# Kernel optimization log

Measured on AMD Instinct MI355X. Metric: run time of the kernel, lower is better.

Reference implementation:

```python
import jax, jax.numpy as jnp
import numpy as np

NUM_REGIONS = 32  # region ids 1..32; id 0 is background, excluded like torch.unique()[ids>0]


def setup_inputs() -> dict:
    key = jax.random.key(0)
    k1, k2 = jax.random.split(key)
    B, T, C, D, H, W = 2, 8, 64, 48, 48, 48
    features = jax.random.normal(k1, (B, T, C, D, H, W), dtype=jnp.float32)
    segmentation = jax.random.randint(k2, (B, 1, D, H, W), 0, NUM_REGIONS + 1, dtype=jnp.int32)
    return {"features": features, "segmentation": segmentation}


def reference(features, segmentation):
    # features: [B, T, C, D, H, W], segmentation: [B, 1, D, H, W] (int region ids)
    B, T, C, D, H, W = features.shape
    N = D * H * W
    seg = segmentation.reshape(B, N)                 # [B, N]
    feats = features.reshape(B, T, C, N)             # [B, T, C, N]

    def per_batch(f, s):
        # f: [T, C, N], s: [N]
        fv = f.reshape(T * C, N).T                   # [N, T*C] voxel-major
        sums = jax.ops.segment_sum(fv, s, num_segments=NUM_REGIONS + 1)          # [R+1, T*C]
        counts = jax.ops.segment_sum(jnp.ones((N,), f.dtype), s,
                                     num_segments=NUM_REGIONS + 1)               # [R+1]
        # mean per region; empty regions stay zero (torch code `continue`s, leaving zeros)
        means = jnp.where(counts[:, None] > 0,
                          sums / jnp.maximum(counts, 1.0)[:, None],
                          0.0)
        return means[1:].reshape(NUM_REGIONS, T, C).transpose(1, 0, 2)           # [T, R, C]

    return jax.vmap(per_batch)(feats, seg)          # [B, T, num_regions, feature_dim]
```

## Files before the change

kernel.cpp:

```cpp
#include <hip/hip_runtime.h>


#define BB 2
#define TT 8
#define CC 64
#define NVOX 110592
#define NREG 32
#define RS 33
#define ACC (RS*CC)
#define CHUNKV 1024
#define VPW (CHUNKV/4)

__global__ __launch_bounds__(256) void seg_hist(const int* __restrict__ seg,
                                                float* __restrict__ counts) {
    __shared__ float h[4 * RS];
    const int tid = threadIdx.x;
    const int w = tid >> 6;
    for (int i = tid; i < 4 * RS; i += 256) h[i] = 0.f;
    __syncthreads();

    const int base = blockIdx.x * 1024 + tid * 4;
    const int b = base / NVOX;
    const int4 s4 = *(const int4*)(seg + base);
    atomicAdd(&h[w * RS + s4.x], 1.f);
    atomicAdd(&h[w * RS + s4.y], 1.f);
    atomicAdd(&h[w * RS + s4.z], 1.f);
    atomicAdd(&h[w * RS + s4.w], 1.f);
    __syncthreads();

    if (tid < RS) {
        const float v = h[tid] + h[RS + tid] + h[2 * RS + tid] + h[3 * RS + tid];
        atomicAdd(&counts[b * RS + tid], v);
    }
}

__global__ __launch_bounds__(256) void seg_sum(const float* __restrict__ feat,
                                               const int* __restrict__ seg,
                                               float* __restrict__ out) {
    __shared__ float s[4 * ACC];
    const int tid = threadIdx.x;
    const int w = tid >> 6;
    const int lane = tid & 63;
    const int b = blockIdx.z;
    const int t = blockIdx.y;

    float* __restrict__ acc = s + w * ACC;
    for (int i = lane; i < ACC; i += 64) acc[i] = 0.f;

    const int v0 = blockIdx.x * CHUNKV + w * VPW;
    const float* __restrict__ fb =
        feat + ((size_t)(b * TT + t) * CC + lane) * NVOX;
    const int* __restrict__ sb = seg + (size_t)b * NVOX;

    #pragma unroll 4
    for (int g = 0; g < VPW; g += 4) {
        const int v = v0 + g;
        const int4 sv = *(const int4*)(sb + v);
        const float4 f = *(const float4*)(fb + v);
        acc[sv.x * CC + lane] += f.x;
        acc[sv.y * CC + lane] += f.y;
        acc[sv.z * CC + lane] += f.z;
        acc[sv.w * CC + lane] += f.w;
    }
    __syncthreads();

    float* __restrict__ outbt = out + (size_t)(b * TT + t) * NREG * CC;
    for (int i = tid; i < NREG * CC; i += 256) {
        const int off = ((i >> 6) + 1) * CC + (i & 63);
        const float v = s[off] + s[ACC + off] + s[2 * ACC + off] + s[3 * ACC + off];
        atomicAdd(&outbt[i], v);
    }
}

__global__ __launch_bounds__(256) void seg_div(float* __restrict__ out,
                                               const float* __restrict__ counts) {
    const int i = blockIdx.x * 256 + threadIdx.x;
    const int b = i >> 14;
    const int r = ((i >> 6) & 31) + 1;
    const float cnt = counts[b * RS + r];
    const float v = out[i];
    out[i] = cnt > 0.f ? v / cnt : 0.f;
}

extern "C" void kernel_launch(void* const* d_in, const int* in_sizes, int n_in,
                              void* d_out, int out_size, void* d_ws, size_t ws_size,
                              hipStream_t stream) {
    const float* feat = (const float*)d_in[0];
    const int* seg = (const int*)d_in[1];
    float* out = (float*)d_out;
    float* counts = (float*)d_ws;

    hipMemsetAsync(d_out, 0, (size_t)out_size * sizeof(float), stream);
    hipMemsetAsync(d_ws, 0, (size_t)(BB * RS) * sizeof(float), stream);

    seg_hist<<<dim3((BB * NVOX) / 1024), 256, 0, stream>>>(seg, counts);
    seg_sum<<<dim3(NVOX / CHUNKV, TT, BB), 256, 0, stream>>>(feat, seg, out);
    seg_div<<<dim3(out_size / 256), 256, 0, stream>>>(out, counts);
}
```

Before: 614.1 us.

## Coalesce feature loads via per-wave LDS transpose tile in segment sum

Each wave now loads 16 consecutive voxels for 16 channels at a time, with 4 lanes per channel, so global reads become contiguous segments instead of one strided row per lane. The values are transposed through a padded per-wave LDS tile, then accumulated into the per-region LDS histogram as before. This targets poor memory coalescing in the bandwidth-bound reduction. The cost is extra LDS traffic and more shared memory per block, which may reduce occupancy.

```diff
diff --git a/kernel.cpp b/kernel.cpp
--- a/kernel.cpp
+++ b/kernel.cpp
@@ -7,9 +7,12 @@
 #define NVOX 110592
 #define NREG 32
 #define RS 33
-#define ACC (RS*CC)
+#define TS 67
+#define WTILE (16*TS)
+#define WACC (RS*CC)
+#define WLDS (WTILE+WACC)
+#define VPW 256
 #define CHUNKV 1024
-#define VPW (CHUNKV/4)
 
 __global__ __launch_bounds__(256) void seg_hist(const int* __restrict__ seg,
                                                 float* __restrict__ counts) {
@@ -37,37 +40,67 @@
 __global__ __launch_bounds__(256) void seg_sum(const float* __restrict__ feat,
                                                const int* __restrict__ seg,
                                                float* __restrict__ out) {
-    __shared__ float s[4 * ACC];
+    __shared__ float s[4 * WLDS];
     const int tid = threadIdx.x;
     const int w = tid >> 6;
-    const int lane = tid & 63;
+    const int l = tid & 63;
     const int b = blockIdx.z;
     const int t = blockIdx.y;
 
-    float* __restrict__ acc = s + w * ACC;
-    for (int i = lane; i < ACC; i += 64) acc[i] = 0.f;
+    float* __restrict__ tile = s + w * WLDS;
+    float* __restrict__ acc = tile + WTILE;
+    #pragma unroll
+    for (int i = l; i < WACC; i += 64) acc[i] = 0.f;
 
     const int v0 = blockIdx.x * CHUNKV + w * VPW;
-    const float* __restrict__ fb =
-        feat + ((size_t)(b * TT + t) * CC + lane) * NVOX;
-    const int* __restrict__ sb = seg + (size_t)b * NVOX;
+    const int cq = l >> 2;
+    const int iq = l & 3;
+    const float* __restrict__ fbt = feat + (size_t)(b * TT + t) * CC * NVOX + v0;
+    const float* __restrict__ fp0 = fbt + (size_t)(cq) * NVOX + iq * 4;
+    const float* __restrict__ fp1 = fbt + (size_t)(cq + 16) * NVOX + iq * 4;
+    const float* __restrict__ fp2 = fbt + (size_t)(cq + 32) * NVOX + iq * 4;
+    const float* __restrict__ fp3 = fbt + (size_t)(cq + 48) * NVOX + iq * 4;
+    const int* __restrict__ sb = seg + (size_t)b * NVOX + v0;
 
-    #pragma unroll 4
-    for (int g = 0; g < VPW; g += 4) {
-        const int v = v0 + g;
-        const int4 sv = *(const int4*)(sb + v);
-        const float4 f = *(const float4*)(fb + v);
-        acc[sv.x * CC + lane] += f.x;
-        acc[sv.y * CC + lane] += f.y;
-        acc[sv.z * CC + lane] += f.z;
-        acc[sv.w * CC + lane] += f.w;
+    const int wb = (iq * 4) * TS + cq;
+
+    #pragma unroll 2
+    for (int tj = 0; tj < 16; ++tj) {
+        const int vo = tj * 16;
+        const float4 f0 = *(const float4*)(fp0 + vo);
+        const float4 f1 = *(const float4*)(fp1 + vo);
+        const float4 f2 = *(const float4*)(fp2 + vo);
+        const float4 f3 = *(const float4*)(fp3 + vo);
+        const int4 s0 = *(const int4*)(sb + vo);
+        const int4 s1 = *(const int4*)(sb + vo + 4);
+        const int4 s2 = *(const int4*)(sb + vo + 8);
+        const int4 s3 = *(const int4*)(sb + vo + 12);
+
+        __builtin_amdgcn_wave_barrier();
+        tile[wb] = f0.x;           tile[wb + TS] = f0.y;
+        tile[wb + 2 * TS] = f0.z;  tile[wb + 3 * TS] = f0.w;
+        tile[wb + 16] = f1.x;          tile[wb + 16 + TS] = f1.y;
+        tile[wb + 16 + 2 * TS] = f1.z; tile[wb + 16 + 3 * TS] = f1.w;
+        tile[wb + 32] = f2.x;          tile[wb + 32 + TS] = f2.y;
+        tile[wb + 32 + 2 * TS] = f2.z; tile[wb + 32 + 3 * TS] = f2.w;
+        tile[wb + 48] = f3.x;          tile[wb + 48 + TS] = f3.y;
+        tile[wb + 48 + 2 * TS] = f3.z; tile[wb + 48 + 3 * TS] = f3.w;
+        __builtin_amdgcn_wave_barrier();
+
+        const int rv[16] = {s0.x, s0.y, s0.z, s0.w, s1.x, s1.y, s1.z, s1.w,
+                            s2.x, s2.y, s2.z, s2.w, s3.x, s3.y, s3.z, s3.w};
+        #pragma unroll
+        for (int v = 0; v < 16; ++v) {
+            const float val = tile[v * TS + l];
+            acc[(rv[v] << 6) + l] += val;
+        }
     }
     __syncthreads();
 
     float* __restrict__ outbt = out + (size_t)(b * TT + t) * NREG * CC;
     for (int i = tid; i < NREG * CC; i += 256) {
-        const int off = ((i >> 6) + 1) * CC + (i & 63);
-        const float v = s[off] + s[ACC + off] + s[2 * ACC + off] + s[3 * ACC + off];
+        const int off = WTILE + ((i >> 6) + 1) * CC + (i & 63);
+        const float v = s[off] + s[WLDS + off] + s[2 * WLDS + off] + s[3 * WLDS + off];
         atomicAdd(&outbt[i], v);
     }
 }
```

New measurement: 613.0 us. No clear change (-0.2%).
